# Kernel tuning notes

Measured on AMD Instinct MI355X. Metric: run time of the kernel, lower is better.

Reference implementation:

```python
import jax, jax.numpy as jnp
import numpy as np

KERNEL = 16
STRIDE = 4


def setup_inputs() -> dict:
    key = jax.random.key(0)
    k1, k2 = jax.random.split(key)
    N, L = 1024, 8192
    inp = jax.random.normal(k1, (N, L), dtype=jnp.float32)
    # nn.init.uniform_(And_weight, 0.3, 0.7)
    And_weight = jax.random.uniform(k2, (1, KERNEL), dtype=jnp.float32, minval=0.3, maxval=0.7)
    return {"input": inp, "And_weight": And_weight}


def reference(input, And_weight):
    N, L = input.shape
    k = And_weight.shape[1]
    starts = jnp.arange(0, L - k + 1, STRIDE)           # [W]
    idx = starts[:, None] + jnp.arange(k)[None, :]       # [W, k]
    windows = input[:, idx]                              # [N, W, k] strided sliding windows
    rho = windows * And_weight[0][None, None, :]         # weighted robustness
    # Temporal_Operators.Always == min over the temporal window (STL 'Always')
    return jnp.min(rho, axis=-1)                         # [N, W]
```

## Files before the change

### kernel.cpp

```cpp
#include <hip/hip_runtime.h>


#define KER 16
#define STR 4
#define ROWLEN 8192
#define NWIN 2045

__global__ __launch_bounds__(256) void and_conv_kernel(
    const float* __restrict__ inp,
    const float* __restrict__ wgt,
    float* __restrict__ out) {
    const int w = blockIdx.x * 256 + threadIdx.x;
    const int n = blockIdx.y;
    if (w >= NWIN) return;

    const float4* row = (const float4*)(inp + (size_t)n * ROWLEN);
    float4 c0 = row[w];
    float4 c1 = row[w + 1];
    float4 c2 = row[w + 2];
    float4 c3 = row[w + 3];

    const float4* wv = (const float4*)wgt;
    float4 w0 = wv[0];
    float4 w1 = wv[1];
    float4 w2 = wv[2];
    float4 w3 = wv[3];

    float m0 = fminf(fminf(c0.x * w0.x, c0.y * w0.y),
                     fminf(c0.z * w0.z, c0.w * w0.w));
    float m1 = fminf(fminf(c1.x * w1.x, c1.y * w1.y),
                     fminf(c1.z * w1.z, c1.w * w1.w));
    float m2 = fminf(fminf(c2.x * w2.x, c2.y * w2.y),
                     fminf(c2.z * w2.z, c2.w * w2.w));
    float m3 = fminf(fminf(c3.x * w3.x, c3.y * w3.y),
                     fminf(c3.z * w3.z, c3.w * w3.w));

    out[(size_t)n * NWIN + w] = fminf(fminf(m0, m1), fminf(m2, m3));
}

extern "C" void kernel_launch(void* const* d_in, const int* in_sizes, int n_in,
                              void* d_out, int out_size, void* d_ws, size_t ws_size,
                              hipStream_t stream) {
    const float* inp = (const float*)d_in[0];
    const float* wgt = (const float*)d_in[1];
    float* out = (float*)d_out;

    const int N = in_sizes[0] / ROWLEN;
    dim3 grid((NWIN + 255) / 256, N);
    and_conv_kernel<<<grid, dim3(256), 0, stream>>>(inp, wgt, out);
}
```

Baseline: 74.81 us.

## Stage each input row in LDS and compute all windows per block

```diff
diff --git a/kernel.cpp b/kernel.cpp
--- a/kernel.cpp
+++ b/kernel.cpp
@@ -1,41 +1,59 @@
 #include <hip/hip_runtime.h>
 
 
-#define KER 16
-#define STR 4
 #define ROWLEN 8192
+#define NCHUNK 2048
 #define NWIN 2045
 
 __global__ __launch_bounds__(256) void and_conv_kernel(
     const float* __restrict__ inp,
     const float* __restrict__ wgt,
     float* __restrict__ out) {
-    const int w = blockIdx.x * 256 + threadIdx.x;
-    const int n = blockIdx.y;
-    if (w >= NWIN) return;
+    __shared__ float4 lds[NCHUNK];
+
+    const int t = threadIdx.x;
+    const int n = blockIdx.x;
 
     const float4* row = (const float4*)(inp + (size_t)n * ROWLEN);
-    float4 c0 = row[w];
-    float4 c1 = row[w + 1];
-    float4 c2 = row[w + 2];
-    float4 c3 = row[w + 3];
+
+#pragma unroll
+    for (int k = 0; k < 8; ++k) {
+        const int g = k * 256 + t;
+        lds[g] = row[g];
+    }
 
     const float4* wv = (const float4*)wgt;
-    float4 w0 = wv[0];
-    float4 w1 = wv[1];
-    float4 w2 = wv[2];
-    float4 w3 = wv[3];
+    const float4 w0 = wv[0];
+    const float4 w1 = wv[1];
+    const float4 w2 = wv[2];
+    const float4 w3 = wv[3];
 
-    float m0 = fminf(fminf(c0.x * w0.x, c0.y * w0.y),
-                     fminf(c0.z * w0.z, c0.w * w0.w));
-    float m1 = fminf(fminf(c1.x * w1.x, c1.y * w1.y),
-                     fminf(c1.z * w1.z, c1.w * w1.w));
-    float m2 = fminf(fminf(c2.x * w2.x, c2.y * w2.y),
-                     fminf(c2.z * w2.z, c2.w * w2.w));
-    float m3 = fminf(fminf(c3.x * w3.x, c3.y * w3.y),
-                     fminf(c3.z * w3.z, c3.w * w3.w));
+    __syncthreads();
 
-    out[(size_t)n * NWIN + w] = fminf(fminf(m0, m1), fminf(m2, m3));
+    float* outrow = out + (size_t)n * NWIN;
+
+#pragma unroll
+    for (int k = 0; k < 8; ++k) {
+        const int w = k * 256 + t;
+        const int wc = (w < NWIN) ? w : (NWIN - 1);
+        const float4 c0 = lds[wc];
+        const float4 c1 = lds[wc + 1];
+        const float4 c2 = lds[wc + 2];
+        const float4 c3 = lds[wc + 3];
+
+        const float m0 = fminf(fminf(c0.x * w0.x, c0.y * w0.y),
+                               fminf(c0.z * w0.z, c0.w * w0.w));
+        const float m1 = fminf(fminf(c1.x * w1.x, c1.y * w1.y),
+                               fminf(c1.z * w1.z, c1.w * w1.w));
+        const float m2 = fminf(fminf(c2.x * w2.x, c2.y * w2.y),
+                               fminf(c2.z * w2.z, c2.w * w2.w));
+        const float m3 = fminf(fminf(c3.x * w3.x, c3.y * w3.y),
+                               fminf(c3.z * w3.z, c3.w * w3.w));
+
+        if (w < NWIN) {
+            outrow[w] = fminf(fminf(m0, m1), fminf(m2, m3));
+        }
+    }
 }
 
 extern "C" void kernel_launch(void* const* d_in, const int* in_sizes, int n_in,
@@ -46,6 +64,5 @@
     float* out = (float*)d_out;
 
     const int N = in_sizes[0] / ROWLEN;
-    dim3 grid((NWIN + 255) / 256, N);
-    and_conv_kernel<<<grid, dim3(256), 0, stream>>>(inp, wgt, out);
+    and_conv_kernel<<<dim3(N), dim3(256), 0, stream>>>(inp, wgt, out);
 }
```

New measurement: 75.87 us. No clear change (+1.4%).
